# Kernel optimization log

Measured on AMD Instinct MI355X. Metric: run time of the kernel, lower is better.

Reference implementation:

```python
import jax, jax.numpy as jnp
import numpy as np
import math

LS = [0, 1, 2]            # degrees present in all irreps
MAX_L = 2
MULT_IN = 64
MULT_MID = 16
MULT_OUT = 64
N = 20000

# ---- Clebsch-Gordan coefficients in the real spherical-harmonic basis ----

def _f(n):
    return math.factorial(int(n))

def _cg_complex(j1, m1, j2, m2, j3, m3):
    if m1 + m2 != m3:
        return 0.0
    pre = math.sqrt((2 * j3 + 1) * _f(j1 + j2 - j3) * _f(j1 - j2 + j3) * _f(-j1 + j2 + j3) / _f(j1 + j2 + j3 + 1))
    pre *= math.sqrt(_f(j1 + m1) * _f(j1 - m1) * _f(j2 + m2) * _f(j2 - m2) * _f(j3 + m3) * _f(j3 - m3))
    kmin = max(0, j2 - j3 - m1, j1 - j3 + m2)
    kmax = min(j1 + j2 - j3, j1 - m1, j2 + m2)
    s = 0.0
    for k in range(kmin, kmax + 1):
        s += (-1) ** k / (_f(k) * _f(j1 + j2 - j3 - k) * _f(j1 - m1 - k) * _f(j2 + m2 - k) * _f(j3 - j2 + m1 + k) * _f(j3 - j1 - m2 + k))
    return pre * s

def _q(l):
    # complex->real change of basis, rows indexed by real m = -l..l
    Q = np.zeros((2 * l + 1, 2 * l + 1), dtype=complex)
    Q[l, l] = 1.0
    r2 = math.sqrt(2.0)
    for m in range(1, l + 1):
        Q[l + m, l + m] = (-1) ** m / r2
        Q[l + m, l - m] = 1.0 / r2
        Q[l - m, l - m] = 1j / r2
        Q[l - m, l + m] = -1j * (-1) ** m / r2
    return Q

def _real_cg(l1, l2, l3):
    C = np.zeros((2 * l1 + 1, 2 * l2 + 1, 2 * l3 + 1), dtype=complex)
    for m1 in range(-l1, l1 + 1):
        for m2 in range(-l2, l2 + 1):
            m3 = m1 + m2
            if -l3 <= m3 <= l3:
                C[l1 + m1, l2 + m2, l3 + m3] = _cg_complex(l1, m1, l2, m2, l3, m3)
    Q1, Q2, Q3 = _q(l1), _q(l2), _q(l3)
    M = np.einsum('ia,jb,kc,abc->ijk', Q1.conj(), Q2.conj(), Q3, C)
    if np.abs(M.imag).max() > np.abs(M.real).max():
        M = M * (-1j)  # fix parity phase so coefficients are real
    assert np.abs(M.imag).max() < 1e-10
    return np.asarray(M.real, dtype=np.float32)

# triangle-rule paths, truncated at MAX_L
PATHS = [(l1, l2, l) for l1 in LS for l2 in LS for l in range(abs(l1 - l2), min(l1 + l2, MAX_L) + 1)]
CG = {p: jnp.asarray(_real_cg(*p)) for p in PATHS}


def setup_inputs() -> dict:
    key = jax.random.key(0)
    ks = jax.random.split(key, 12)
    inp = {}
    for i, l in enumerate(LS):
        inp[f'x{l}'] = jax.random.normal(ks[i], (N, MULT_IN, 2 * l + 1), dtype=jnp.float32)
    for i, l in enumerate(LS):
        inp[f'W1_{l}'] = jax.random.normal(ks[3 + i], (MULT_IN, MULT_MID), dtype=jnp.float32)
        inp[f'W2_{l}'] = jax.random.normal(ks[6 + i], (MULT_IN, MULT_MID), dtype=jnp.float32)
    tp_mults = {l: sum(MULT_MID * MULT_MID for (l1, l2, lo) in PATHS if lo == l) for l in LS}
    for i, l in enumerate(LS):
        inp[f'W3_{l}'] = jax.random.normal(ks[9 + i], (tp_mults[l], MULT_OUT), dtype=jnp.float32)
    return inp


def _linear(x, W):
    # x: [n, u, i], W: [u, v] -> [n, v, i], normalized like e3nn Linear
    return jnp.einsum('nui,uv->nvi', x, W) / np.float32(math.sqrt(x.shape[1]))


def reference(x0, x1, x2, W1_0, W1_1, W1_2, W2_0, W2_1, W2_2, W3_0, W3_1, W3_2):
    xs = [x0, x1, x2]
    W1 = [W1_0, W1_1, W1_2]
    W2 = [W2_0, W2_1, W2_2]
    W3 = [W3_0, W3_1, W3_2]
    a = [_linear(xs[l], W1[l]) for l in LS]   # branch 1
    b = [_linear(xs[l], W2[l]) for l in LS]   # branch 2
    # CG tensor product up to MAX_L, full (uv) multiplicity
    tp = {l: [] for l in LS}
    n = x0.shape[0]
    for (l1, l2, l) in PATHS:
        t = jnp.einsum('nui,nvj,ijk->nuvk', a[l1], b[l2], CG[(l1, l2, l)])
        tp[l].append(t.reshape(n, MULT_MID * MULT_MID, 2 * l + 1))
    outs = []
    for l in LS:
        z = jnp.concatenate(tp[l], axis=1)        # [n, tp_mult_l, 2l+1]
        y = _linear(z, W3[l])                     # [n, MULT_OUT, 2l+1]
        outs.append(y.reshape(n, -1))
    return jnp.concatenate(outs, axis=1)          # [n, MULT_OUT * 9]
```

## Files before the change

### kernel.cpp

```cpp
#include <hip/hip_runtime.h>


typedef __attribute__((ext_vector_type(4))) float f32x4;
typedef __attribute__((ext_vector_type(4))) float f4;
typedef __attribute__((ext_vector_type(2))) float f2;
typedef __attribute__((ext_vector_type(8))) short short8;
typedef unsigned short ushort_t;
typedef unsigned int uint32;

__device__ __forceinline__ uint32 bfb(float x) {
  uint32 u = __float_as_uint(x);
  return (u + 0x7fffu + ((u >> 16) & 1u)) >> 16;
}
__device__ __forceinline__ uint32 pack2f(f2 z) {
  uint32 lo = __float_as_uint(z.x) + 0x8000u;
  uint32 hi = __float_as_uint(z.y) + 0x8000u;
  return __builtin_amdgcn_perm(hi, lo, 0x07060302u);
}

#define C2   0.7071067811865476f
#define C3   0.5773502691896258f
#define C5   0.4472135954999579f
#define C6   0.4082482904638631f
#define C23  0.8164965809277260f
#define C10  0.3162277660168379f
#define C210 0.6324555320336759f
#define C310 0.5477225575051661f
#define C14  0.2672612419124244f
#define C214 0.5345224838248488f
#define C314 0.4629100498862757f

__global__ __launch_bounds__(256) void pack_w3_kernel(
    const float* __restrict__ W30, const float* __restrict__ W31,
    const float* __restrict__ W32, ushort_t* __restrict__ pack) {
  int lc = blockIdx.x;
  int t = threadIdx.x >> 6;
  int lam = threadIdx.x & 63;
  const float* W;
  int mb;
  float nrm;
  if (lc < 24) {
    W = W30; mb = lc * 32; nrm = 0.036084391824351615f;
  } else if (lc < 72) {
    W = W31; mb = (lc - 24) * 32; nrm = 0.025515518153991442f;
  } else {
    W = W32; mb = (lc - 72) * 32; nrm = 0.025515518153991442f;
  }
  int w = t * 16 + (lam & 15);
  int m0 = mb + (lam >> 4) * 8;
  ushort_t* dst = pack + ((size_t)(lc * 4 + t) * 64 + lam) * 8;
#pragma unroll
  for (int j = 0; j < 8; ++j)
    dst[j] = (ushort_t)bfb(W[(size_t)(m0 + j) * 64 + w] * nrm);
}

template <int NK, int JD, class F>
__device__ __forceinline__ void zgenv(const float* bsj, ushort_t* zrow, F f) {
  uint32 zp[NK][8];
#pragma unroll
  for (int oc = 0; oc < 2; ++oc) {
    f2 bb4[JD][4];
#pragma unroll
    for (int j = 0; j < JD; ++j) {
      f4 lo = *(const f4*)(bsj + j * 16 + oc * 8);
      f4 hi = *(const f4*)(bsj + j * 16 + oc * 8 + 4);
      bb4[j][0] = lo.xy; bb4[j][1] = lo.zw;
      bb4[j][2] = hi.xy; bb4[j][3] = hi.zw;
    }
#pragma unroll
    for (int q = 0; q < 4; ++q) {
      f2 bcol[JD], z[NK];
#pragma unroll
      for (int j = 0; j < JD; ++j) bcol[j] = bb4[j][q];
      f(bcol, z);
#pragma unroll
      for (int k = 0; k < NK; ++k) zp[k][oc * 4 + q] = pack2f(z[k]);
    }
  }
#pragma unroll
  for (int k = 0; k < NK; ++k) {
    uint32* d = (uint32*)(zrow + k * (16 * 264));
    *(uint4*)(d) = make_uint4(zp[k][0], zp[k][1], zp[k][2], zp[k][3]);
    *(uint4*)(d + 4) = make_uint4(zp[k][4], zp[k][5], zp[k][6], zp[k][7]);
  }
}

template <int NROW>
__device__ __forceinline__ void mfma2(const ushort_t* zb, const ushort_t* pk,
                                      int pcbase, int h, int wt0, int lane,
                                      f32x4* accA, f32x4* accB) {
  const int srow = lane & 15, quad = lane >> 4;
  const ushort_t* ab = zb + srow * 264 + quad * 8 + h * 128;
  const ushort_t* bb = pk + ((size_t)((pcbase + h * 4) * 4 + wt0) * 64 + lane) * 8;
#pragma unroll
  for (int c = 0; c < 4; ++c) {
    short8 B0 = *(const short8*)(bb + (size_t)c * 2048);
    short8 B1 = *(const short8*)(bb + (size_t)c * 2048 + 512);
#pragma unroll
    for (int rt = 0; rt < NROW; ++rt) {
      short8 A = *(const short8*)(ab + rt * (16 * 264) + c * 32);
      accA[rt] = __builtin_amdgcn_mfma_f32_16x16x32_bf16(A, B0, accA[rt], 0, 0, 0);
      accB[rt] = __builtin_amdgcn_mfma_f32_16x16x32_bf16(A, B1, accB[rt], 0, 0, 0);
    }
  }
}

#define ZB 12672

__global__ __launch_bounds__(256, 2) void tdense_kernel(
    const float* __restrict__ x0, const float* __restrict__ x1,
    const float* __restrict__ x2, const float* __restrict__ W10,
    const float* __restrict__ W20, const float* __restrict__ W11,
    const float* __restrict__ W21, const float* __restrict__ W12,
    const float* __restrict__ W22, const ushort_t* __restrict__ pack,
    float* __restrict__ out) {
  __shared__ float b_s[2368];
  __shared__ __align__(16) ushort_t zbuf[2 * ZB];

  const int tid = threadIdx.x;
  const int nbase = blockIdx.x * 16;
  const int s = tid >> 4, v = tid & 15;

  const int n = nbase + s;
  const float* px0 = x0 + (size_t)n * 64;
  const float* px1 = x1 + (size_t)n * 192;
  const float* px2 = x2 + (size_t)n * 320;
  float a0 = 0.f, a1x = 0.f, a1y = 0.f, a1z = 0.f;
  float a2[5] = {0.f, 0.f, 0.f, 0.f, 0.f};
  float b0 = 0.f, b1x = 0.f, b1y = 0.f, b1z = 0.f;
  float b2[5] = {0.f, 0.f, 0.f, 0.f, 0.f};
  for (int u4 = 0; u4 < 16; ++u4) {
    f4 xv0 = *(const f4*)(px0 + u4 * 4);
    f4 xa = *(const f4*)(px1 + u4 * 12);
    f4 xb = *(const f4*)(px1 + u4 * 12 + 4);
    f4 xc = *(const f4*)(px1 + u4 * 12 + 8);
    f4 ya = *(const f4*)(px2 + u4 * 20);
    f4 yb = *(const f4*)(px2 + u4 * 20 + 4);
    f4 yc = *(const f4*)(px2 + u4 * 20 + 8);
    f4 yd = *(const f4*)(px2 + u4 * 20 + 12);
    f4 ye = *(const f4*)(px2 + u4 * 20 + 16);
    float x1e[12], x2e[20];
#pragma unroll
    for (int e = 0; e < 4; ++e) { x1e[e] = xa[e]; x1e[4 + e] = xb[e]; x1e[8 + e] = xc[e]; }
#pragma unroll
    for (int e = 0; e < 4; ++e) {
      x2e[e] = ya[e]; x2e[4 + e] = yb[e]; x2e[8 + e] = yc[e];
      x2e[12 + e] = yd[e]; x2e[16 + e] = ye[e];
    }
#pragma unroll
    for (int r = 0; r < 4; ++r) {
      int u = u4 * 4 + r;
      float wa0 = W10[u * 16 + v], wb0 = W20[u * 16 + v];
      float wa1 = W11[u * 16 + v], wb1 = W21[u * 16 + v];
      float wa2 = W12[u * 16 + v], wb2 = W22[u * 16 + v];
      float xx = xv0[r];
      a0 += xx * wa0; b0 += xx * wb0;
      float e0 = x1e[r * 3 + 0], e1 = x1e[r * 3 + 1], e2 = x1e[r * 3 + 2];
      a1x += e0 * wa1; a1y += e1 * wa1; a1z += e2 * wa1;
      b1x += e0 * wb1; b1y += e1 * wb1; b1z += e2 * wb1;
#pragma unroll
      for (int j = 0; j < 5; ++j) {
        float ev = x2e[r * 5 + j];
        a2[j] += ev * wa2;
        b2[j] += ev * wb2;
      }
    }
  }
  const float inv8 = 0.125f;
  float ar[9];
  ar[0] = a0 * inv8;
  ar[1] = a1x * inv8; ar[2] = a1y * inv8; ar[3] = a1z * inv8;
#pragma unroll
  for (int j = 0; j < 5; ++j) ar[4 + j] = a2[j] * inv8;
  {
    float* bw = b_s + s * 148 + v;
    bw[0] = b0 * inv8;
    bw[16] = b1x * inv8; bw[32] = b1y * inv8; bw[48] = b1z * inv8;
#pragma unroll
    for (int j = 0; j < 5; ++j) bw[64 + j * 16] = b2[j] * inv8;
  }

  const int lane = tid & 63;
  const int wv = tid >> 6;
  const int p2 = (wv & 1) * 2;
  const int h = wv >> 1;

  f32x4 aA0, aB0, aA1[3], aB1[3], aA2[5], aB2[5];
  aA0 = (f32x4)(0.f); aB0 = (f32x4)(0.f);
#pragma unroll
  for (int i = 0; i < 3; ++i) { aA1[i] = (f32x4)(0.f); aB1[i] = (f32x4)(0.f); }
#pragma unroll
  for (int i = 0; i < 5; ++i) { aA2[i] = (f32x4)(0.f); aB2[i] = (f32x4)(0.f); }

  const float* bsl0 = b_s + s * 148;
  const float* bsl1 = bsl0 + 16;
  const float* bsl2 = bsl0 + 64;
  ushort_t* z0 = zbuf + s * 264 + v * 16;
  ushort_t* z1 = z0 + ZB;
  const ushort_t* Zb0 = zbuf;
  const ushort_t* Zb1 = zbuf + ZB;

  zgenv<1, 1>(bsl0, z0, [&](const f2* b, f2* z) { z[0] = ar[0] * b[0]; });
  zgenv<1, 3>(bsl1, z0 + 4224, [&](const f2* b, f2* z) {
    z[0] = -C3 * (ar[1] * b[0] + ar[2] * b[1] + ar[3] * b[2]);
  });
  zgenv<1, 5>(bsl2, z0 + 8448, [&](const f2* b, f2* z) {
    z[0] = C5 * (ar[4] * b[0] + ar[5] * b[1] + ar[6] * b[2] + ar[7] * b[3] + ar[8] * b[4]);
  });
  __syncthreads();

  zgenv<3, 3>(bsl1, z1, [&](const f2* b, f2* z) {
    z[0] = ar[0] * b[0]; z[1] = ar[0] * b[1]; z[2] = ar[0] * b[2];
  });
  mfma2<1>(Zb0, pack, 0, h, p2, lane, &aA0, &aB0);
  mfma2<1>(Zb0 + 4224, pack, 8, h, p2, lane, &aA0, &aB0);
  mfma2<1>(Zb0 + 8448, pack, 16, h, p2, lane, &aA0, &aB0);
  __syncthreads();

  zgenv<3, 1>(bsl0, z0, [&](const f2* b, f2* z) {
    z[0] = ar[1] * b[0]; z[1] = ar[2] * b[0]; z[2] = ar[3] * b[0];
  });
  mfma2<3>(Zb1, pack, 24, h, p2, lane, aA1, aB1);
  __syncthreads();

  zgenv<3, 3>(bsl1, z1, [&](const f2* b, f2* z) {
    z[0] = C2 * (ar[2] * b[2] - ar[3] * b[1]);
    z[1] = C2 * (ar[3] * b[0] - ar[1] * b[2]);
    z[2] = C2 * (ar[1] * b[1] - ar[2] * b[0]);
  });
  mfma2<3>(Zb0, pack, 32, h, p2, lane, aA1, aB1);
  __syncthreads();

  zgenv<3, 5>(bsl2, z0, [&](const f2* b, f2* z) {
    z[0] = -C310 * ar[2] * b[1] + C10 * ar[1] * b[2] - C310 * ar[3] * b[0] + C310 * ar[1] * b[4];
    z[1] = -C210 * ar[2] * b[2] - C310 * ar[3] * b[3] - C310 * ar[1] * b[1];
    z[2] = -C310 * ar[2] * b[3] + C10 * ar[3] * b[2] - C310 * ar[1] * b[0] - C310 * ar[3] * b[4];
  });
  mfma2<3>(Zb1, pack, 40, h, p2, lane, aA1, aB1);
  __syncthreads();

  zgenv<3, 3>(bsl1, z1, [&](const f2* b, f2* z) {
    z[0] = -C310 * ar[5] * b[1] + C10 * ar[6] * b[0] - C310 * ar[4] * b[2] + C310 * ar[8] * b[0];
    z[1] = -C210 * ar[6] * b[1] - C310 * ar[7] * b[2] - C310 * ar[5] * b[0];
    z[2] = -C310 * ar[7] * b[1] + C10 * ar[6] * b[2] - C310 * ar[4] * b[0] - C310 * ar[8] * b[2];
  });
  mfma2<3>(Zb0, pack, 48, h, p2, lane, aA1, aB1);
  __syncthreads();

  zgenv<3, 5>(bsl2, z0, [&](const f2* b, f2* z) {
    z[0] = C10 * (ar[8] * b[3] - ar[7] * b[4] + ar[4] * b[1] - ar[5] * b[0]) +
           C310 * (ar[7] * b[2] - ar[6] * b[3]);
    z[1] = C10 * (ar[5] * b[3] - ar[7] * b[1]) + C210 * (ar[4] * b[4] - ar[8] * b[0]);
    z[2] = C10 * (ar[8] * b[1] - ar[5] * b[4] + ar[7] * b[0] - ar[4] * b[3]) +
           C310 * (ar[6] * b[1] - ar[5] * b[2]);
  });
  mfma2<3>(Zb1, pack, 56, h, p2, lane, aA1, aB1);
  __syncthreads();

  zgenv<3, 5>(bsl2, z1, [&](const f2* b, f2* z) {
    z[0] = ar[0] * b[0]; z[1] = ar[0] * b[1]; z[2] = ar[0] * b[2];
  });
  mfma2<3>(Zb0, pack, 64, h, p2, lane, aA1, aB1);
  __syncthreads();

  zgenv<2, 5>(bsl2, z0, [&](const f2* b, f2* z) {
    z[0] = ar[0] * b[3]; z[1] = ar[0] * b[4];
  });
  mfma2<3>(Zb1, pack, 72, h, p2, lane, aA2, aB2);
  __syncthreads();

  zgenv<3, 3>(bsl1, z1, [&](const f2* b, f2* z) {
    z[0] = C2 * (ar[1] * b[2] + ar[3] * b[0]);
    z[1] = C2 * (ar[2] * b[0] + ar[1] * b[1]);
    z[2] = C23 * ar[2] * b[1] - C6 * (ar[1] * b[0] + ar[3] * b[2]);
  });
  mfma2<2>(Zb0, pack, 72, h, p2, lane, aA2 + 3, aB2 + 3);
  __syncthreads();

  zgenv<2, 3>(bsl1, z0, [&](const f2* b, f2* z) {
    z[0] = C2 * (ar[2] * b[2] + ar[3] * b[1]);
    z[1] = C2 * (ar[3] * b[2] - ar[1] * b[0]);
  });
  mfma2<3>(Zb1, pack, 80, h, p2, lane, aA2, aB2);
  __syncthreads();

  zgenv<3, 5>(bsl2, z1, [&](const f2* b, f2* z) {
    z[0] = C23 * ar[2] * b[4] + C6 * ar[1] * b[1] - C6 * ar[3] * b[3];
    z[1] = C6 * ar[2] * b[3] - C6 * ar[1] * b[0] - C2 * ar[3] * b[2] - C6 * ar[3] * b[4];
    z[2] = C2 * (ar[3] * b[1] - ar[1] * b[3]);
  });
  mfma2<2>(Zb0, pack, 80, h, p2, lane, aA2 + 3, aB2 + 3);
  __syncthreads();

  zgenv<2, 5>(bsl2, z0, [&](const f2* b, f2* z) {
    z[0] = -C6 * ar[2] * b[1] + C2 * ar[1] * b[2] + C6 * ar[3] * b[0] - C6 * ar[1] * b[4];
    z[1] = -C23 * ar[2] * b[0] + C6 * ar[1] * b[3] + C6 * ar[3] * b[1];
  });
  mfma2<3>(Zb1, pack, 88, h, p2, lane, aA2, aB2);
  __syncthreads();

  zgenv<3, 1>(bsl0, z1, [&](const f2* b, f2* z) {
    z[0] = ar[4] * b[0]; z[1] = ar[5] * b[0]; z[2] = ar[6] * b[0];
  });
  mfma2<2>(Zb0, pack, 88, h, p2, lane, aA2 + 3, aB2 + 3);
  __syncthreads();

  zgenv<2, 1>(bsl0, z0, [&](const f2* b, f2* z) {
    z[0] = ar[7] * b[0]; z[1] = ar[8] * b[0];
  });
  mfma2<3>(Zb1, pack, 96, h, p2, lane, aA2, aB2);
  __syncthreads();

  zgenv<3, 3>(bsl1, z1, [&](const f2* b, f2* z) {
    z[0] = -C23 * ar[8] * b[1] - C6 * ar[5] * b[0] + C6 * ar[7] * b[2];
    z[1] = -C6 * ar[7] * b[1] + C6 * ar[4] * b[0] + C2 * ar[6] * b[2] + C6 * ar[8] * b[2];
    z[2] = C2 * (ar[7] * b[0] - ar[5] * b[2]);
  });
  mfma2<2>(Zb0, pack, 96, h, p2, lane, aA2 + 3, aB2 + 3);
  __syncthreads();

  zgenv<2, 3>(bsl1, z0, [&](const f2* b, f2* z) {
    z[0] = C6 * ar[5] * b[1] - C2 * ar[6] * b[0] - C6 * ar[4] * b[2] + C6 * ar[8] * b[0];
    z[1] = C23 * ar[4] * b[1] - C6 * ar[7] * b[0] - C6 * ar[5] * b[2];
  });
  mfma2<3>(Zb1, pack, 104, h, p2, lane, aA2, aB2);
  __syncthreads();

  zgenv<3, 5>(bsl2, z1, [&](const f2* b, f2* z) {
    z[0] = C214 * (ar[6] * b[0] + ar[4] * b[2]) - C314 * (ar[5] * b[3] + ar[7] * b[1]);
    z[1] = -C14 * (ar[6] * b[1] + ar[5] * b[2]) + C314 * (ar[5] * b[4] + ar[8] * b[1]) -
           C314 * (ar[7] * b[0] + ar[4] * b[3]);
    z[2] = -C214 * ar[6] * b[2] - C14 * (ar[5] * b[1] + ar[7] * b[3]) +
           C214 * (ar[4] * b[0] + ar[8] * b[4]);
  });
  mfma2<2>(Zb0, pack, 104, h, p2, lane, aA2 + 3, aB2 + 3);
  __syncthreads();

  zgenv<2, 5>(bsl2, z0, [&](const f2* b, f2* z) {
    z[0] = -C14 * (ar[6] * b[3] + ar[7] * b[2]) - C314 * (ar[5] * b[0] + ar[4] * b[1]) -
           C314 * (ar[7] * b[4] + ar[8] * b[3]);
    z[1] = C214 * (ar[6] * b[4] + ar[8] * b[2]) + C314 * (ar[5] * b[1] - ar[7] * b[3]);
  });
  mfma2<3>(Zb1, pack, 112, h, p2, lane, aA2, aB2);
  __syncthreads();

  mfma2<2>(Zb0, pack, 112, h, p2, lane, aA2 + 3, aB2 + 3);
  __syncthreads();

  float* red = (float*)zbuf;
  const int col = lane & 15, quad = lane >> 4;
  if (h == 0) {
#pragma unroll
    for (int pp = 0; pp < 2; ++pp) {
      int wt = p2 + pp;
      const f32x4* src0 = pp ? &aB0 : &aA0;
      const f32x4* src1 = pp ? aB1 : aA1;
      const f32x4* src2 = pp ? aB2 : aA2;
      *(f4*)(red + (wt * 9 + 0) * 256 + lane * 4) = src0[0];
#pragma unroll
      for (int o = 0; o < 3; ++o)
        *(f4*)(red + (wt * 9 + 1 + o) * 256 + lane * 4) = src1[o];
#pragma unroll
      for (int o = 0; o < 5; ++o)
        *(f4*)(red + (wt * 9 + 4 + o) * 256 + lane * 4) = src2[o];
    }
  }
  __syncthreads();
  if (h == 1) {
    aA0 += *(const f4*)(red + (p2 * 9 + 0) * 256 + lane * 4);
    aB0 += *(const f4*)(red + ((p2 + 1) * 9 + 0) * 256 + lane * 4);
#pragma unroll
    for (int o = 0; o < 3; ++o) {
      aA1[o] += *(const f4*)(red + (p2 * 9 + 1 + o) * 256 + lane * 4);
      aB1[o] += *(const f4*)(red + ((p2 + 1) * 9 + 1 + o) * 256 + lane * 4);
    }
#pragma unroll
    for (int o = 0; o < 5; ++o) {
      aA2[o] += *(const f4*)(red + (p2 * 9 + 4 + o) * 256 + lane * 4);
      aB2[o] += *(const f4*)(red + ((p2 + 1) * 9 + 4 + o) * 256 + lane * 4);
    }
    const int w0 = p2 * 16 + col, w1 = w0 + 16;
#pragma unroll
    for (int r = 0; r < 4; ++r) {
      int so = quad * 4 + r;
      float* row = out + (size_t)(nbase + so) * 576;
      row[w0] = aA0[r];
      row[w1] = aB0[r];
      row[64 + w0 * 3 + 0] = aA1[0][r];
      row[64 + w0 * 3 + 1] = aA1[1][r];
      row[64 + w0 * 3 + 2] = aA1[2][r];
      row[64 + w1 * 3 + 0] = aB1[0][r];
      row[64 + w1 * 3 + 1] = aB1[1][r];
      row[64 + w1 * 3 + 2] = aB1[2][r];
#pragma unroll
      for (int k = 0; k < 5; ++k) {
        row[256 + w0 * 5 + k] = aA2[k][r];
        row[256 + w1 * 5 + k] = aB2[k][r];
      }
    }
  }
}

extern "C" void kernel_launch(void* const* d_in, const int* in_sizes, int n_in,
                              void* d_out, int out_size, void* d_ws, size_t ws_size,
                              hipStream_t stream) {
  const float* x0 = (const float*)d_in[0];
  const float* x1 = (const float*)d_in[1];
  const float* x2 = (const float*)d_in[2];
  const float* W10 = (const float*)d_in[3];
  const float* W20 = (const float*)d_in[4];
  const float* W11 = (const float*)d_in[5];
  const float* W21 = (const float*)d_in[6];
  const float* W12 = (const float*)d_in[7];
  const float* W22 = (const float*)d_in[8];
  const float* W30 = (const float*)d_in[9];
  const float* W31 = (const float*)d_in[10];
  const float* W32 = (const float*)d_in[11];
  ushort_t* pack = (ushort_t*)d_ws;

  hipLaunchKernelGGL(pack_w3_kernel, dim3(120), dim3(256), 0, stream,
                     W30, W31, W32, pack);

  int nsamp = in_sizes[0] / 64;
  int nblocks = nsamp / 16;
  hipLaunchKernelGGL(tdense_kernel, dim3(nblocks), dim3(256), 0, stream,
                     x0, x1, x2, W10, W20, W11, W21, W12, W22, pack,
                     (float*)d_out);
}
```

Before: 218.9 us.

## Shrink LDS z-buffers to raise occupancy and transpose W1/W2 for vector loads

The double-buffered z staging area in shared memory is cut from two 3-slot buffers to a 3-slot plus 2-slot layout, and the tensor-product chunks are rescheduled so each stage fills at most that many slots. This lowers LDS use enough to allow three blocks per CU instead of two, which is meant to improve latency hiding. The first-layer weights are also pre-transposed by an extra block in the packing kernel, so each thread can read them as float4 vectors instead of strided scalars. In exchange there are more, smaller MFMA/sync stages, each with its own barrier, and register pressure rises under the tighter launch bound.

```diff
diff --git a/kernel.cpp b/kernel.cpp
--- a/kernel.cpp
+++ b/kernel.cpp
@@ -32,8 +32,20 @@
 
 __global__ __launch_bounds__(256) void pack_w3_kernel(
     const float* __restrict__ W30, const float* __restrict__ W31,
-    const float* __restrict__ W32, ushort_t* __restrict__ pack) {
+    const float* __restrict__ W32, const float* __restrict__ W10,
+    const float* __restrict__ W11, const float* __restrict__ W12,
+    const float* __restrict__ W20, const float* __restrict__ W21,
+    const float* __restrict__ W22, ushort_t* __restrict__ pack,
+    float* __restrict__ Wt) {
   int lc = blockIdx.x;
+  if (lc == 120) {
+    const float* Ws[6] = {W10, W11, W12, W20, W21, W22};
+    for (int idx = threadIdx.x; idx < 6144; idx += 256) {
+      int u = idx & 63, v = (idx >> 6) & 15, li = idx >> 10;
+      Wt[idx] = Ws[li][u * 16 + v];
+    }
+    return;
+  }
   int t = threadIdx.x >> 6;
   int lam = threadIdx.x & 63;
   const float* W;
@@ -105,17 +117,15 @@
   }
 }
 
-#define ZB 12672
-
-__global__ __launch_bounds__(256, 2) void tdense_kernel(
+#define SLOT 4224
+#define ZBOFF 12672
+
+__global__ __launch_bounds__(256, 3) void tdense_kernel(
     const float* __restrict__ x0, const float* __restrict__ x1,
-    const float* __restrict__ x2, const float* __restrict__ W10,
-    const float* __restrict__ W20, const float* __restrict__ W11,
-    const float* __restrict__ W21, const float* __restrict__ W12,
-    const float* __restrict__ W22, const ushort_t* __restrict__ pack,
-    float* __restrict__ out) {
+    const float* __restrict__ x2, const float* __restrict__ Wt,
+    const ushort_t* __restrict__ pack, float* __restrict__ out) {
   __shared__ float b_s[2368];
-  __shared__ __align__(16) ushort_t zbuf[2 * ZB];
+  __shared__ __align__(16) ushort_t zbuf[21120];
 
   const int tid = threadIdx.x;
   const int nbase = blockIdx.x * 16;
@@ -125,6 +135,12 @@
   const float* px0 = x0 + (size_t)n * 64;
   const float* px1 = x1 + (size_t)n * 192;
   const float* px2 = x2 + (size_t)n * 320;
+  const float* wa0p = Wt + (0 * 16 + v) * 64;
+  const float* wa1p = Wt + (1 * 16 + v) * 64;
+  const float* wa2p = Wt + (2 * 16 + v) * 64;
+  const float* wb0p = Wt + (3 * 16 + v) * 64;
+  const float* wb1p = Wt + (4 * 16 + v) * 64;
+  const float* wb2p = Wt + (5 * 16 + v) * 64;
   float a0 = 0.f, a1x = 0.f, a1y = 0.f, a1z = 0.f;
   float a2[5] = {0.f, 0.f, 0.f, 0.f, 0.f};
   float b0 = 0.f, b1x = 0.f, b1y = 0.f, b1z = 0.f;
@@ -139,6 +155,12 @@
     f4 yc = *(const f4*)(px2 + u4 * 20 + 8);
     f4 yd = *(const f4*)(px2 + u4 * 20 + 12);
     f4 ye = *(const f4*)(px2 + u4 * 20 + 16);
+    f4 wA0 = *(const f4*)(wa0p + u4 * 4);
+    f4 wA1 = *(const f4*)(wa1p + u4 * 4);
+    f4 wA2 = *(const f4*)(wa2p + u4 * 4);
+    f4 wB0 = *(const f4*)(wb0p + u4 * 4);
+    f4 wB1 = *(const f4*)(wb1p + u4 * 4);
+    f4 wB2 = *(const f4*)(wb2p + u4 * 4);
     float x1e[12], x2e[20];
 #pragma unroll
     for (int e = 0; e < 4; ++e) { x1e[e] = xa[e]; x1e[4 + e] = xb[e]; x1e[8 + e] = xc[e]; }
@@ -149,20 +171,16 @@
     }
 #pragma unroll
     for (int r = 0; r < 4; ++r) {
-      int u = u4 * 4 + r;
-      float wa0 = W10[u * 16 + v], wb0 = W20[u * 16 + v];
-      float wa1 = W11[u * 16 + v], wb1 = W21[u * 16 + v];
-      float wa2 = W12[u * 16 + v], wb2 = W22[u * 16 + v];
       float xx = xv0[r];
-      a0 += xx * wa0; b0 += xx * wb0;
+      a0 += xx * wA0[r]; b0 += xx * wB0[r];
       float e0 = x1e[r * 3 + 0], e1 = x1e[r * 3 + 1], e2 = x1e[r * 3 + 2];
-      a1x += e0 * wa1; a1y += e1 * wa1; a1z += e2 * wa1;
-      b1x += e0 * wb1; b1y += e1 * wb1; b1z += e2 * wb1;
+      a1x += e0 * wA1[r]; a1y += e1 * wA1[r]; a1z += e2 * wA1[r];
+      b1x += e0 * wB1[r]; b1y += e1 * wB1[r]; b1z += e2 * wB1[r];
 #pragma unroll
       for (int j = 0; j < 5; ++j) {
         float ev = x2e[r * 5 + j];
-        a2[j] += ev * wa2;
-        b2[j] += ev * wb2;
+        a2[j] += ev * wA2[r];
+        b2[j] += ev * wB2[r];
       }
     }
   }
@@ -195,156 +213,189 @@
   const float* bsl0 = b_s + s * 148;
   const float* bsl1 = bsl0 + 16;
   const float* bsl2 = bsl0 + 64;
-  ushort_t* z0 = zbuf + s * 264 + v * 16;
-  ushort_t* z1 = z0 + ZB;
-  const ushort_t* Zb0 = zbuf;
-  const ushort_t* Zb1 = zbuf + ZB;
-
-  zgenv<1, 1>(bsl0, z0, [&](const f2* b, f2* z) { z[0] = ar[0] * b[0]; });
-  zgenv<1, 3>(bsl1, z0 + 4224, [&](const f2* b, f2* z) {
+  ushort_t* zA = zbuf + s * 264 + v * 16;
+  ushort_t* zB = zA + ZBOFF;
+  const ushort_t* ZA = zbuf;
+  const ushort_t* ZB = zbuf + ZBOFF;
+
+  zgenv<1, 1>(bsl0, zA, [&](const f2* b, f2* z) { z[0] = ar[0] * b[0]; });
+  zgenv<1, 3>(bsl1, zA + SLOT, [&](const f2* b, f2* z) {
     z[0] = -C3 * (ar[1] * b[0] + ar[2] * b[1] + ar[3] * b[2]);
   });
-  zgenv<1, 5>(bsl2, z0 + 8448, [&](const f2* b, f2* z) {
+  zgenv<1, 5>(bsl2, zA + 2 * SLOT, [&](const f2* b, f2* z) {
     z[0] = C5 * (ar[4] * b[0] + ar[5] * b[1] + ar[6] * b[2] + ar[7] * b[3] + ar[8] * b[4]);
   });
   __syncthreads();
 
-  zgenv<3, 3>(bsl1, z1, [&](const f2* b, f2* z) {
-    z[0] = ar[0] * b[0]; z[1] = ar[0] * b[1]; z[2] = ar[0] * b[2];
-  });
-  mfma2<1>(Zb0, pack, 0, h, p2, lane, &aA0, &aB0);
-  mfma2<1>(Zb0 + 4224, pack, 8, h, p2, lane, &aA0, &aB0);
-  mfma2<1>(Zb0 + 8448, pack, 16, h, p2, lane, &aA0, &aB0);
-  __syncthreads();
-
-  zgenv<3, 1>(bsl0, z0, [&](const f2* b, f2* z) {
-    z[0] = ar[1] * b[0]; z[1] = ar[2] * b[0]; z[2] = ar[3] * b[0];
-  });
-  mfma2<3>(Zb1, pack, 24, h, p2, lane, aA1, aB1);
-  __syncthreads();
-
-  zgenv<3, 3>(bsl1, z1, [&](const f2* b, f2* z) {
+  zgenv<2, 3>(bsl1, zB, [&](const f2* b, f2* z) {
+    z[0] = ar[0] * b[0]; z[1] = ar[0] * b[1];
+  });
+  mfma2<1>(ZA, pack, 0, h, p2, lane, &aA0, &aB0);
+  mfma2<1>(ZA + SLOT, pack, 8, h, p2, lane, &aA0, &aB0);
+  mfma2<1>(ZA + 2 * SLOT, pack, 16, h, p2, lane, &aA0, &aB0);
+  __syncthreads();
+
+  zgenv<1, 3>(bsl1, zA, [&](const f2* b, f2* z) { z[0] = ar[0] * b[2]; });
+  zgenv<2, 1>(bsl0, zA + SLOT, [&](const f2* b, f2* z) {
+    z[0] = ar[1] * b[0]; z[1] = ar[2] * b[0];
+  });
+  mfma2<2>(ZB, pack, 24, h, p2, lane, aA1, aB1);
+  __syncthreads();
+
+  zgenv<1, 1>(bsl0, zB, [&](const f2* b, f2* z) { z[0] = ar[3] * b[0]; });
+  zgenv<1, 3>(bsl1, zB + SLOT, [&](const f2* b, f2* z) {
     z[0] = C2 * (ar[2] * b[2] - ar[3] * b[1]);
-    z[1] = C2 * (ar[3] * b[0] - ar[1] * b[2]);
-    z[2] = C2 * (ar[1] * b[1] - ar[2] * b[0]);
-  });
-  mfma2<3>(Zb0, pack, 32, h, p2, lane, aA1, aB1);
-  __syncthreads();
-
-  zgenv<3, 5>(bsl2, z0, [&](const f2* b, f2* z) {
+  });
+  mfma2<1>(ZA, pack, 24, h, p2, lane, aA1 + 2, aB1 + 2);
+  mfma2<2>(ZA + SLOT, pack, 32, h, p2, lane, aA1, aB1);
+  __syncthreads();
+
+  zgenv<2, 3>(bsl1, zA, [&](const f2* b, f2* z) {
+    z[0] = C2 * (ar[3] * b[0] - ar[1] * b[2]);
+    z[1] = C2 * (ar[1] * b[1] - ar[2] * b[0]);
+  });
+  zgenv<1, 5>(bsl2, zA + 2 * SLOT, [&](const f2* b, f2* z) {
     z[0] = -C310 * ar[2] * b[1] + C10 * ar[1] * b[2] - C310 * ar[3] * b[0] + C310 * ar[1] * b[4];
-    z[1] = -C210 * ar[2] * b[2] - C310 * ar[3] * b[3] - C310 * ar[1] * b[1];
-    z[2] = -C310 * ar[2] * b[3] + C10 * ar[3] * b[2] - C310 * ar[1] * b[0] - C310 * ar[3] * b[4];
-  });
-  mfma2<3>(Zb1, pack, 40, h, p2, lane, aA1, aB1);
-  __syncthreads();
-
-  zgenv<3, 3>(bsl1, z1, [&](const f2* b, f2* z) {
+  });
+  mfma2<1>(ZB, pack, 32, h, p2, lane, aA1 + 2, aB1 + 2);
+  mfma2<1>(ZB + SLOT, pack, 40, h, p2, lane, aA1, aB1);
+  __syncthreads();
+
+  zgenv<2, 5>(bsl2, zB, [&](const f2* b, f2* z) {
+    z[0] = -C210 * ar[2] * b[2] - C310 * ar[3] * b[3] - C310 * ar[1] * b[1];
+    z[1] = -C310 * ar[2] * b[3] + C10 * ar[3] * b[2] - C310 * ar[1] * b[0] - C310 * ar[3] * b[4];
+  });
+  mfma2<2>(ZA, pack, 40, h, p2, lane, aA1 + 1, aB1 + 1);
+  mfma2<1>(ZA + 2 * SLOT, pack, 48, h, p2, lane, aA1, aB1);
+  __syncthreads();
+
+  zgenv<3, 3>(bsl1, zA, [&](const f2* b, f2* z) {
     z[0] = -C310 * ar[5] * b[1] + C10 * ar[6] * b[0] - C310 * ar[4] * b[2] + C310 * ar[8] * b[0];
     z[1] = -C210 * ar[6] * b[1] - C310 * ar[7] * b[2] - C310 * ar[5] * b[0];
     z[2] = -C310 * ar[7] * b[1] + C10 * ar[6] * b[2] - C310 * ar[4] * b[0] - C310 * ar[8] * b[2];
   });
-  mfma2<3>(Zb0, pack, 48, h, p2, lane, aA1, aB1);
-  __syncthreads();
-
-  zgenv<3, 5>(bsl2, z0, [&](const f2* b, f2* z) {
+  mfma2<2>(ZB, pack, 48, h, p2, lane, aA1 + 1, aB1 + 1);
+  __syncthreads();
+
+  zgenv<2, 5>(bsl2, zB, [&](const f2* b, f2* z) {
     z[0] = C10 * (ar[8] * b[3] - ar[7] * b[4] + ar[4] * b[1] - ar[5] * b[0]) +
            C310 * (ar[7] * b[2] - ar[6] * b[3]);
     z[1] = C10 * (ar[5] * b[3] - ar[7] * b[1]) + C210 * (ar[4] * b[4] - ar[8] * b[0]);
-    z[2] = C10 * (ar[8] * b[1] - ar[5] * b[4] + ar[7] * b[0] - ar[4] * b[3]) +
+  });
+  mfma2<3>(ZA, pack, 56, h, p2, lane, aA1, aB1);
+  __syncthreads();
+
+  zgenv<1, 5>(bsl2, zA, [&](const f2* b, f2* z) {
+    z[0] = C10 * (ar[8] * b[1] - ar[5] * b[4] + ar[7] * b[0] - ar[4] * b[3]) +
            C310 * (ar[6] * b[1] - ar[5] * b[2]);
   });
-  mfma2<3>(Zb1, pack, 56, h, p2, lane, aA1, aB1);
-  __syncthreads();
-
-  zgenv<3, 5>(bsl2, z1, [&](const f2* b, f2* z) {
-    z[0] = ar[0] * b[0]; z[1] = ar[0] * b[1]; z[2] = ar[0] * b[2];
-  });
-  mfma2<3>(Zb0, pack, 64, h, p2, lane, aA1, aB1);
-  __syncthreads();
-
-  zgenv<2, 5>(bsl2, z0, [&](const f2* b, f2* z) {
-    z[0] = ar[0] * b[3]; z[1] = ar[0] * b[4];
-  });
-  mfma2<3>(Zb1, pack, 72, h, p2, lane, aA2, aB2);
-  __syncthreads();
-
-  zgenv<3, 3>(bsl1, z1, [&](const f2* b, f2* z) {
+  zgenv<2, 5>(bsl2, zA + SLOT, [&](const f2* b, f2* z) {
+    z[0] = ar[0] * b[0]; z[1] = ar[0] * b[1];
+  });
+  mfma2<2>(ZB, pack, 64, h, p2, lane, aA1, aB1);
+  __syncthreads();
+
+  zgenv<2, 5>(bsl2, zB, [&](const f2* b, f2* z) {
+    z[0] = ar[0] * b[2]; z[1] = ar[0] * b[3];
+  });
+  mfma2<1>(ZA, pack, 64, h, p2, lane, aA1 + 2, aB1 + 2);
+  mfma2<2>(ZA + SLOT, pack, 72, h, p2, lane, aA2, aB2);
+  __syncthreads();
+
+  zgenv<1, 5>(bsl2, zA, [&](const f2* b, f2* z) { z[0] = ar[0] * b[4]; });
+  zgenv<2, 3>(bsl1, zA + SLOT, [&](const f2* b, f2* z) {
     z[0] = C2 * (ar[1] * b[2] + ar[3] * b[0]);
     z[1] = C2 * (ar[2] * b[0] + ar[1] * b[1]);
-    z[2] = C23 * ar[2] * b[1] - C6 * (ar[1] * b[0] + ar[3] * b[2]);
-  });
-  mfma2<2>(Zb0, pack, 72, h, p2, lane, aA2 + 3, aB2 + 3);
-  __syncthreads();
-
-  zgenv<2, 3>(bsl1, z0, [&](const f2* b, f2* z) {
-    z[0] = C2 * (ar[2] * b[2] + ar[3] * b[1]);
-    z[1] = C2 * (ar[3] * b[2] - ar[1] * b[0]);
-  });
-  mfma2<3>(Zb1, pack, 80, h, p2, lane, aA2, aB2);
-  __syncthreads();
-
-  zgenv<3, 5>(bsl2, z1, [&](const f2* b, f2* z) {
+  });
+  mfma2<2>(ZB, pack, 72, h, p2, lane, aA2 + 2, aB2 + 2);
+  __syncthreads();
+
+  zgenv<2, 3>(bsl1, zB, [&](const f2* b, f2* z) {
+    z[0] = C23 * ar[2] * b[1] - C6 * (ar[1] * b[0] + ar[3] * b[2]);
+    z[1] = C2 * (ar[2] * b[2] + ar[3] * b[1]);
+  });
+  mfma2<1>(ZA, pack, 72, h, p2, lane, aA2 + 4, aB2 + 4);
+  mfma2<2>(ZA + SLOT, pack, 80, h, p2, lane, aA2, aB2);
+  __syncthreads();
+
+  zgenv<1, 3>(bsl1, zA, [&](const f2* b, f2* z) {
+    z[0] = C2 * (ar[3] * b[2] - ar[1] * b[0]);
+  });
+  zgenv<2, 5>(bsl2, zA + SLOT, [&](const f2* b, f2* z) {
     z[0] = C23 * ar[2] * b[4] + C6 * ar[1] * b[1] - C6 * ar[3] * b[3];
     z[1] = C6 * ar[2] * b[3] - C6 * ar[1] * b[0] - C2 * ar[3] * b[2] - C6 * ar[3] * b[4];
-    z[2] = C2 * (ar[3] * b[1] - ar[1] * b[3]);
-  });
-  mfma2<2>(Zb0, pack, 80, h, p2, lane, aA2 + 3, aB2 + 3);
-  __syncthreads();
-
-  zgenv<2, 5>(bsl2, z0, [&](const f2* b, f2* z) {
-    z[0] = -C6 * ar[2] * b[1] + C2 * ar[1] * b[2] + C6 * ar[3] * b[0] - C6 * ar[1] * b[4];
-    z[1] = -C23 * ar[2] * b[0] + C6 * ar[1] * b[3] + C6 * ar[3] * b[1];
-  });
-  mfma2<3>(Zb1, pack, 88, h, p2, lane, aA2, aB2);
-  __syncthreads();
-
-  zgenv<3, 1>(bsl0, z1, [&](const f2* b, f2* z) {
-    z[0] = ar[4] * b[0]; z[1] = ar[5] * b[0]; z[2] = ar[6] * b[0];
-  });
-  mfma2<2>(Zb0, pack, 88, h, p2, lane, aA2 + 3, aB2 + 3);
-  __syncthreads();
-
-  zgenv<2, 1>(bsl0, z0, [&](const f2* b, f2* z) {
-    z[0] = ar[7] * b[0]; z[1] = ar[8] * b[0];
-  });
-  mfma2<3>(Zb1, pack, 96, h, p2, lane, aA2, aB2);
-  __syncthreads();
-
-  zgenv<3, 3>(bsl1, z1, [&](const f2* b, f2* z) {
+  });
+  mfma2<2>(ZB, pack, 80, h, p2, lane, aA2 + 2, aB2 + 2);
+  __syncthreads();
+
+  zgenv<2, 5>(bsl2, zB, [&](const f2* b, f2* z) {
+    z[0] = C2 * (ar[3] * b[1] - ar[1] * b[3]);
+    z[1] = -C6 * ar[2] * b[1] + C2 * ar[1] * b[2] + C6 * ar[3] * b[0] - C6 * ar[1] * b[4];
+  });
+  mfma2<1>(ZA, pack, 80, h, p2, lane, aA2 + 4, aB2 + 4);
+  mfma2<2>(ZA + SLOT, pack, 88, h, p2, lane, aA2, aB2);
+  __syncthreads();
+
+  zgenv<1, 5>(bsl2, zA, [&](const f2* b, f2* z) {
+    z[0] = -C23 * ar[2] * b[0] + C6 * ar[1] * b[3] + C6 * ar[3] * b[1];
+  });
+  zgenv<2, 1>(bsl0, zA + SLOT, [&](const f2* b, f2* z) {
+    z[0] = ar[4] * b[0]; z[1] = ar[5] * b[0];
+  });
+  mfma2<2>(ZB, pack, 88, h, p2, lane, aA2 + 2, aB2 + 2);
+  __syncthreads();
+
+  zgenv<2, 1>(bsl0, zB, [&](const f2* b, f2* z) {
+    z[0] = ar[6] * b[0]; z[1] = ar[7] * b[0];
+  });
+  mfma2<1>(ZA, pack, 88, h, p2, lane, aA2 + 4, aB2 + 4);
+  mfma2<2>(ZA + SLOT, pack, 96, h, p2, lane, aA2, aB2);
+  __syncthreads();
+
+  zgenv<1, 1>(bsl0, zA, [&](const f2* b, f2* z) { z[0] = ar[8] * b[0]; });
+  zgenv<2, 3>(bsl1, zA + SLOT, [&](const f2* b, f2* z) {
     z[0] = -C23 * ar[8] * b[1] - C6 * ar[5] * b[0] + C6 * ar[7] * b[2];
     z[1] = -C6 * ar[7] * b[1] + C6 * ar[4] * b[0] + C2 * ar[6] * b[2] + C6 * ar[8] * b[2];
-    z[2] = C2 * (ar[7] * b[0] - ar[5] * b[2]);
-  });
-  mfma2<2>(Zb0, pack, 96, h, p2, lane, aA2 + 3, aB2 + 3);
-  __syncthreads();
-
-  zgenv<2, 3>(bsl1, z0, [&](const f2* b, f2* z) {
-    z[0] = C6 * ar[5] * b[1] - C2 * ar[6] * b[0] - C6 * ar[4] * b[2] + C6 * ar[8] * b[0];
-    z[1] = C23 * ar[4] * b[1] - C6 * ar[7] * b[0] - C6 * ar[5] * b[2];
-  });
-  mfma2<3>(Zb1, pack, 104, h, p2, lane, aA2, aB2);
-  __syncthreads();
-
-  zgenv<3, 5>(bsl2, z1, [&](const f2* b, f2* z) {
+  });
+  mfma2<2>(ZB, pack, 96, h, p2, lane, aA2 + 2, aB2 + 2);
+  __syncthreads();
+
+  zgenv<2, 3>(bsl1, zB, [&](const f2* b, f2* z) {
+    z[0] = C2 * (ar[7] * b[0] - ar[5] * b[2]);
+    z[1] = C6 * ar[5] * b[1] - C2 * ar[6] * b[0] - C6 * ar[4] * b[2] + C6 * ar[8] * b[0];
+  });
+  mfma2<1>(ZA, pack, 96, h, p2, lane, aA2 + 4, aB2 + 4);
+  mfma2<2>(ZA + SLOT, pack, 104, h, p2, lane, aA2, aB2);
+  __syncthreads();
+
+  zgenv<1, 3>(bsl1, zA, [&](const f2* b, f2* z) {
+    z[0] = C23 * ar[4] * b[1] - C6 * ar[7] * b[0] - C6 * ar[5] * b[2];
+  });
+  zgenv<2, 5>(bsl2, zA + SLOT, [&](const f2* b, f2* z) {
     z[0] = C214 * (ar[6] * b[0] + ar[4] * b[2]) - C314 * (ar[5] * b[3] + ar[7] * b[1]);
     z[1] = -C14 * (ar[6] * b[1] + ar[5] * b[2]) + C314 * (ar[5] * b[4] + ar[8] * b[1]) -
            C314 * (ar[7] * b[0] + ar[4] * b[3]);
-    z[2] = -C214 * ar[6] * b[2] - C14 * (ar[5] * b[1] + ar[7] * b[3]) +
+  });
+  mfma2<2>(ZB, pack, 104, h, p2, lane, aA2 + 2, aB2 + 2);
+  __syncthreads();
+
+  zgenv<2, 5>(bsl2, zB, [&](const f2* b, f2* z) {
+    z[0] = -C214 * ar[6] * b[2] - C14 * (ar[5] * b[1] + ar[7] * b[3]) +
            C214 * (ar[4] * b[0] + ar[8] * b[4]);
-  });
-  mfma2<2>(Zb0, pack, 104, h, p2, lane, aA2 + 3, aB2 + 3);
-  __syncthreads();
-
-  zgenv<2, 5>(bsl2, z0, [&](const f2* b, f2* z) {
-    z[0] = -C14 * (ar[6] * b[3] + ar[7] * b[2]) - C314 * (ar[5] * b[0] + ar[4] * b[1]) -
+    z[1] = -C14 * (ar[6] * b[3] + ar[7] * b[2]) - C314 * (ar[5] * b[0] + ar[4] * b[1]) -
            C314 * (ar[7] * b[4] + ar[8] * b[3]);
-    z[1] = C214 * (ar[6] * b[4] + ar[8] * b[2]) + C314 * (ar[5] * b[1] - ar[7] * b[3]);
-  });
-  mfma2<3>(Zb1, pack, 112, h, p2, lane, aA2, aB2);
-  __syncthreads();
-
-  mfma2<2>(Zb0, pack, 112, h, p2, lane, aA2 + 3, aB2 + 3);
+  });
+  mfma2<1>(ZA, pack, 104, h, p2, lane, aA2 + 4, aB2 + 4);
+  mfma2<2>(ZA + SLOT, pack, 112, h, p2, lane, aA2, aB2);
+  __syncthreads();
+
+  zgenv<1, 5>(bsl2, zA, [&](const f2* b, f2* z) {
+    z[0] = C214 * (ar[6] * b[4] + ar[8] * b[2]) + C314 * (ar[5] * b[1] - ar[7] * b[3]);
+  });
+  mfma2<2>(ZB, pack, 112, h, p2, lane, aA2 + 2, aB2 + 2);
+  __syncthreads();
+
+  mfma2<1>(ZA, pack, 112, h, p2, lane, aA2 + 4, aB2 + 4);
   __syncthreads();
 
   float* red = (float*)zbuf;
@@ -417,13 +468,13 @@
   const float* W31 = (const float*)d_in[10];
   const float* W32 = (const float*)d_in[11];
   ushort_t* pack = (ushort_t*)d_ws;
-
-  hipLaunchKernelGGL(pack_w3_kernel, dim3(120), dim3(256), 0, stream,
-                     W30, W31, W32, pack);
+  float* Wt = (float*)((char*)d_ws + 491520);
+
+  hipLaunchKernelGGL(pack_w3_kernel, dim3(121), dim3(256), 0, stream,
+                     W30, W31, W32, W10, W11, W12, W20, W21, W22, pack, Wt);
 
   int nsamp = in_sizes[0] / 64;
   int nblocks = nsamp / 16;
   hipLaunchKernelGGL(tdense_kernel, dim3(nblocks), dim3(256), 0, stream,
-                     x0, x1, x2, W10, W20, W11, W21, W12, W22, pack,
-                     (float*)d_out);
-}
+                     x0, x1, x2, Wt, pack, (float*)d_out);
+}
```

After: 245.9 us. +12.3%, slower.
